# Optimization experiments

Measured on AMD Instinct MI355X. Metric: run time of the kernel, lower is better.

The kernel has to match this reference:

```python
import jax, jax.numpy as jnp
import numpy as np

N = 131072
MANO_CHILD = (2, 3, 17, 5, 6, 18, 8, 9, 20, 11, 12, 19, 14, 15, 16)
MANO_PARENT = (1, 2, 3, 4, 5, 6, 7, 8, 9, 10, 11, 12, 13, 14, 15)
FINGERS = ((0, 1, 2, 3, 17), (0, 4, 5, 6, 18), (0, 7, 8, 9, 20), (0, 10, 11, 12, 19), (0, 13, 14, 15, 16))
PALM = np.array([0, 1, 4, 7, 10, 13])
MAX_FLEX = float(np.pi / 2)  # flexion clamp range [0, pi/2]
EPS = 1e-8


def _wrist_rot(src, dst):
    """Kabsch rotation R (N,3,3) such that R @ src_k ~= dst_k (palm alignment)."""
    H = jnp.einsum('nki,nkj->nij', src, dst)          # sum_k src dst^T
    U, S, Vt = jnp.linalg.svd(H, full_matrices=False)
    VUt = jnp.einsum('nji,nkj->nik', Vt, U)           # V @ U^T
    d = jnp.linalg.det(VUt)
    D = jnp.stack([jnp.ones_like(d), jnp.ones_like(d), d], axis=-1)
    return jnp.einsum('nji,nj,nkj->nik', Vt, D, U)    # V diag(1,1,d) U^T


def _rodrigues(v, axis, theta):
    """Rotate vectors v (N,3) about unit axis (N,3) by angle theta (N,)."""
    c = jnp.cos(theta)[:, None]
    s = jnp.sin(theta)[:, None]
    return v * c + jnp.cross(axis, v) * s + axis * jnp.sum(axis * v, -1, keepdims=True) * (1.0 - c)


def _forward(joints, tempJ):
    wrist = joints[:, :1]
    J = joints - wrist                       # wrist-centered observed joints
    T = tempJ - tempJ[:, :1]                 # wrist-centered template
    bone_ref = T                             # bonelenTempJ: reference bone lengths
    # rigid palm alignment of template onto observed joints
    R = _wrist_rot(T[:, PALM], J[:, PALM])
    T = jnp.einsum('nij,nkj->nki', R, T)     # rotate every template joint
    # palm joints of observation are replaced by aligned template palm
    J = J.at[:, PALM].set(T[:, PALM])
    # (hand-pose-legitimize layer approximated as identity; source unavailable)
    for idx in range(len(MANO_CHILD)):
        ch, pa = MANO_CHILD[idx], MANO_PARENT[idx]
        v1 = J[:, ch] - T[:, pa]
        dis = jnp.linalg.norm(v1, axis=1)
        univ1 = v1 / (dis[:, None] + EPS)
        blen = jnp.linalg.norm(bone_ref[:, ch] - bone_ref[:, pa], axis=1)
        lo, hi = blen, blen                  # non-RHD template: lower == upper
        valid = (lo <= dis) & (dis <= hi)
        clamped = jnp.clip(dis, lo, hi)
        new = jnp.where(valid[:, None], J[:, ch], T[:, pa] + univ1 * clamped[:, None])
        T = T.at[:, ch].set(new)
        # flexion legitimization: clamp bend angle of this bone vs its parent bone
        f = FINGERS[idx // 3]
        k = idx % 3
        gp, pp, cc = f[k], f[k + 1], f[k + 2]  # grandparent, parent(=pa), child(=ch)
        v0 = T[:, pp] - T[:, gp]
        vb = T[:, cc] - T[:, pp]
        cr = jnp.cross(v0, vb)
        s = jnp.linalg.norm(cr, axis=1)
        c = jnp.sum(v0 * vb, axis=1)
        ang = jnp.arctan2(s, c)
        delta = jnp.clip(ang, 0.0, MAX_FLEX) - ang
        axis = cr / (s[:, None] + EPS)
        T = T.at[:, cc].set(_rodrigues(vb, axis, delta) + T[:, pp])
    return wrist + T


def setup_inputs() -> dict:
    key = jax.random.key(0)
    k1, k2 = jax.random.split(key)
    joints = jax.random.normal(k1, (N, 21, 3), dtype=jnp.float32)
    tempJ = jax.random.normal(k2, (N, 21, 3), dtype=jnp.float32)
    return {"joints": joints, "tempJ": tempJ}


def reference(joints, tempJ):
    return _forward(joints, tempJ)
```

## Files before the change

kernel.cpp:

```cpp
#include <hip/hip_runtime.h>
#include <math.h>

#define BLOCK 256
#define HF 63
#define TILE_F (BLOCK * HF)
#define TILE_V4 (TILE_F / 4)

__device__ __forceinline__ float rsqf(float x)  { return __builtin_amdgcn_rsqf(x); }
__device__ __forceinline__ float sqtf(float x)  { return __builtin_amdgcn_sqrtf(x); }

__global__ __launch_bounds__(BLOCK, 2)
void kin_fwd(const float* __restrict__ joints,
             const float* __restrict__ tempJ,
             float* __restrict__ out,
             int n_total)
{
    constexpr int CHILD[15]  = {2,3,17, 5,6,18, 8,9,20, 11,12,19, 14,15,16};
    constexpr int PARENT[15] = {1,2,3, 4,5,6, 7,8,9, 10,11,12, 13,14,15};
    constexpr int GPID[15]   = {0,1,2, 0,4,5, 0,7,8, 0,10,11, 0,13,14};
    constexpr int PALM[6]    = {0,1,4,7,10,13};

    __shared__ float lds[TILE_F];

    const int tid = threadIdx.x;
    const int n   = blockIdx.x * BLOCK + tid;
    const long long tileBase = (long long)blockIdx.x * TILE_F;
    const long long totalF   = (long long)n_total * HF;
    const bool fullTile = (tileBase + TILE_F) <= totalF;
    const bool active = (n < n_total);

    if (fullTile) {
        const float4* g4 = (const float4*)(tempJ + tileBase);
        float4* l4 = (float4*)lds;
        for (int idx = tid; idx < TILE_V4; idx += BLOCK) l4[idx] = g4[idx];
    } else {
        for (int idx = tid; idx < TILE_F; idx += BLOCK) {
            const long long g = tileBase + idx;
            lds[idx] = (g < totalF) ? tempJ[g] : 0.f;
        }
    }
    __syncthreads();

    float T[21][3];
    float blen2[15];

    if (active) {
        const float* tl = lds + tid * HF;
#pragma unroll
        for (int k = 0; k < 21; ++k) {
            T[k][0] = tl[3*k+0];
            T[k][1] = tl[3*k+1];
            T[k][2] = tl[3*k+2];
        }
        const float ox = T[0][0], oy = T[0][1], oz = T[0][2];
#pragma unroll
        for (int k = 0; k < 21; ++k) { T[k][0] -= ox; T[k][1] -= oy; T[k][2] -= oz; }

#pragma unroll
        for (int i = 0; i < 15; ++i) {
            const float dx = T[CHILD[i]][0] - T[PARENT[i]][0];
            const float dy = T[CHILD[i]][1] - T[PARENT[i]][1];
            const float dz = T[CHILD[i]][2] - T[PARENT[i]][2];
            blen2[i] = dx*dx + dy*dy + dz*dz;
        }
    }
    __syncthreads();

    if (fullTile) {
        const float4* g4 = (const float4*)(joints + tileBase);
        float4* l4 = (float4*)lds;
        for (int idx = tid; idx < TILE_V4; idx += BLOCK) l4[idx] = g4[idx];
    } else {
        for (int idx = tid; idx < TILE_F; idx += BLOCK) {
            const long long g = tileBase + idx;
            lds[idx] = (g < totalF) ? joints[g] : 0.f;
        }
    }
    __syncthreads();

    float wx = 0.f, wy = 0.f, wz = 0.f;

    if (active) {
        float Jl[21][3];
        {
            const float* jl = lds + tid * HF;
            wx = jl[0]; wy = jl[1]; wz = jl[2];
#pragma unroll
            for (int k = 0; k < 21; ++k) {
                Jl[k][0] = jl[3*k+0] - wx;
                Jl[k][1] = jl[3*k+1] - wy;
                Jl[k][2] = jl[3*k+2] - wz;
            }
        }

        float H[3][3] = {{0.f,0.f,0.f},{0.f,0.f,0.f},{0.f,0.f,0.f}};
#pragma unroll
        for (int p = 0; p < 6; ++p) {
            const int k = PALM[p];
#pragma unroll
            for (int i = 0; i < 3; ++i)
#pragma unroll
                for (int j = 0; j < 3; ++j)
                    H[i][j] += T[k][i] * Jl[k][j];
        }

        float A[3][3];
#pragma unroll
        for (int i = 0; i < 3; ++i)
#pragma unroll
            for (int j = 0; j < 3; ++j)
                A[i][j] = H[0][i]*H[0][j] + H[1][i]*H[1][j] + H[2][i]*H[2][j];

        const float q   = (A[0][0] + A[1][1] + A[2][2]) * (1.f/3.f);
        const float a00 = A[0][0]-q, a11 = A[1][1]-q, a22 = A[2][2]-q;
        const float a01 = A[0][1], a02 = A[0][2], a12 = A[1][2];
        const float p1  = a01*a01 + a02*a02 + a12*a12;
        const float p2s = a00*a00 + a11*a11 + a22*a22 + 2.f*p1;
        const float p26 = p2s*(1.f/6.f) + 1e-30f;
        const float ip  = rsqf(p26);
        const float p   = p26 * ip;
        const float detC =
            a00*(a11*a22 - a12*a12) - a01*(a01*a22 - a12*a02) + a02*(a01*a12 - a11*a02);
        float r = 0.5f * detC * ip*ip*ip;
        r = fminf(1.f, fmaxf(-1.f, r));
        const float phi_rev = acosf(r) * 0.05305164769729845f;
        const float cph = __builtin_amdgcn_cosf(phi_rev);
        const float sph = __builtin_amdgcn_sinf(phi_rev);
        const float e1 = q + 2.f*p*cph;
        const float e3 = q - p*(cph + 1.7320508075688772f*sph);
        const float e2 = 3.f*q - e1 - e3;

        const float gap12 = e1 - e2, gap23 = e2 - e3;
        const bool isoTop = (gap12 >= gap23);
        const float sAB = isoTop ? (e2 + e3) : (e1 + e2);
        const float pAB = isoTop ? (e2 * e3) : (e1 * e2);

        const float A2_00 = A[0][0]*A[0][0] + A[0][1]*A[0][1] + A[0][2]*A[0][2];
        const float A2_01 = A[0][0]*A[0][1] + A[0][1]*A[1][1] + A[0][2]*A[1][2];
        const float A2_02 = A[0][0]*A[0][2] + A[0][1]*A[1][2] + A[0][2]*A[2][2];
        const float A2_11 = A[0][1]*A[0][1] + A[1][1]*A[1][1] + A[1][2]*A[1][2];
        const float A2_12 = A[0][1]*A[0][2] + A[1][1]*A[1][2] + A[1][2]*A[2][2];
        const float A2_22 = A[0][2]*A[0][2] + A[1][2]*A[1][2] + A[2][2]*A[2][2];

        const float m00 = A2_00 - sAB*A[0][0] + pAB;
        const float m01 = A2_01 - sAB*A[0][1];
        const float m02 = A2_02 - sAB*A[0][2];
        const float m11 = A2_11 - sAB*A[1][1] + pAB;
        const float m12 = A2_12 - sAB*A[1][2];
        const float m22 = A2_22 - sAB*A[2][2] + pAB;

        const float n0c = m00*m00 + m01*m01 + m02*m02;
        const float n1c = m01*m01 + m11*m11 + m12*m12;
        const float n2c = m02*m02 + m12*m12 + m22*m22;
        float vx = m00, vy = m01, vz = m02, nb = n0c;
        if (n1c > nb) { vx = m01; vy = m11; vz = m12; nb = n1c; }
        if (n2c > nb) { vx = m02; vy = m12; vz = m22; nb = n2c; }
        if (nb < 1e-24f) { vx = 1.f; vy = 0.f; vz = 0.f; }
        {
            const float invv = rsqf(vx*vx + vy*vy + vz*vz + 1e-35f);
            vx *= invv; vy *= invv; vz *= invv;
        }

        float hx, hy, hz;
        {
            const float axv = fabsf(vx), ayv = fabsf(vy), azv = fabsf(vz);
            if (axv <= ayv && axv <= azv)      { hx = 0.f;  hy = vz;  hz = -vy; }
            else if (ayv <= azv)               { hx = -vz;  hy = 0.f; hz = vx;  }
            else                               { hx = vy;   hy = -vx; hz = 0.f; }
        }
        const float invh = rsqf(hx*hx + hy*hy + hz*hz + 1e-35f);
        const float b1x = hx*invh, b1y = hy*invh, b1z = hz*invh;
        const float b2x = vy*b1z - vz*b1y;
        const float b2y = vz*b1x - vx*b1z;
        const float b2z = vx*b1y - vy*b1x;

        const float Ab1x = A[0][0]*b1x + A[0][1]*b1y + A[0][2]*b1z;
        const float Ab1y = A[0][1]*b1x + A[1][1]*b1y + A[1][2]*b1z;
        const float Ab1z = A[0][2]*b1x + A[1][2]*b1y + A[2][2]*b1z;
        const float Ab2x = A[0][0]*b2x + A[0][1]*b2y + A[0][2]*b2z;
        const float Ab2y = A[0][1]*b2x + A[1][1]*b2y + A[1][2]*b2z;
        const float Ab2z = A[0][2]*b2x + A[1][2]*b2y + A[2][2]*b2z;
        const float alpha = b1x*Ab1x + b1y*Ab1y + b1z*Ab1z;
        const float beta  = b2x*Ab1x + b2y*Ab1y + b2z*Ab1z;
        const float gamma = b2x*Ab2x + b2y*Ab2y + b2z*Ab2z;

        const float difq  = 0.5f*(alpha - gamma);
        const float rootq = sqtf(difq*difq + beta*beta);
        float tx = beta, ty = rootq - difq;
        if (tx*tx + ty*ty < 1e-30f) { tx = 1.f; ty = 0.f; }
        const float invt = rsqf(tx*tx + ty*ty + 1e-35f);
        const float ctx = tx*invt, cty = ty*invt;
        const float wpx = ctx*b1x + cty*b2x;
        const float wpy = ctx*b1y + cty*b2y;
        const float wpz = ctx*b1z + cty*b2z;
        const float wmx = vy*wpz - vz*wpy;
        const float wmy = vz*wpx - vx*wpz;
        const float wmz = vx*wpy - vy*wpx;

        const float v1x = isoTop ? vx  : wpx;
        const float v1y = isoTop ? vy  : wpy;
        const float v1z = isoTop ? vz  : wpz;
        const float v2x = isoTop ? wpx : wmx;
        const float v2y = isoTop ? wpy : wmy;
        const float v2z = isoTop ? wpz : wmz;
        const float v3x = v1y*v2z - v1z*v2y;
        const float v3y = v1z*v2x - v1x*v2z;
        const float v3z = v1x*v2y - v1y*v2x;

        float R[3][3];
        {
            const float w1x = H[0][0]*v1x + H[0][1]*v1y + H[0][2]*v1z;
            const float w1y = H[1][0]*v1x + H[1][1]*v1y + H[1][2]*v1z;
            const float w1z = H[2][0]*v1x + H[2][1]*v1y + H[2][2]*v1z;
            const float in1 = rsqf(w1x*w1x + w1y*w1y + w1z*w1z + 1e-35f);
            const float u1x = w1x*in1, u1y = w1y*in1, u1z = w1z*in1;

            float w2x = H[0][0]*v2x + H[0][1]*v2y + H[0][2]*v2z;
            float w2y = H[1][0]*v2x + H[1][1]*v2y + H[1][2]*v2z;
            float w2z = H[2][0]*v2x + H[2][1]*v2y + H[2][2]*v2z;
            const float dp = u1x*w2x + u1y*w2y + u1z*w2z;
            w2x -= dp*u1x; w2y -= dp*u1y; w2z -= dp*u1z;
            const float in2 = rsqf(w2x*w2x + w2y*w2y + w2z*w2z + 1e-35f);
            const float u2x = w2x*in2, u2y = w2y*in2, u2z = w2z*in2;

            const float u3x = u1y*u2z - u1z*u2y;
            const float u3y = u1z*u2x - u1x*u2z;
            const float u3z = u1x*u2y - u1y*u2x;

            R[0][0] = v1x*u1x + v2x*u2x + v3x*u3x;
            R[0][1] = v1x*u1y + v2x*u2y + v3x*u3y;
            R[0][2] = v1x*u1z + v2x*u2z + v3x*u3z;
            R[1][0] = v1y*u1x + v2y*u2x + v3y*u3x;
            R[1][1] = v1y*u1y + v2y*u2y + v3y*u3y;
            R[1][2] = v1y*u1z + v2y*u2z + v3y*u3z;
            R[2][0] = v1z*u1x + v2z*u2x + v3z*u3x;
            R[2][1] = v1z*u1y + v2z*u2y + v3z*u3y;
            R[2][2] = v1z*u1z + v2z*u2z + v3z*u3z;
        }

#pragma unroll
        for (int k = 0; k < 21; ++k) {
            const float x = T[k][0], y = T[k][1], z = T[k][2];
            T[k][0] = R[0][0]*x + R[0][1]*y + R[0][2]*z;
            T[k][1] = R[1][0]*x + R[1][1]*y + R[1][2]*z;
            T[k][2] = R[2][0]*x + R[2][1]*y + R[2][2]*z;
        }

#pragma unroll
        for (int i = 0; i < 15; ++i) {
            const int ch = CHILD[i], pa = PARENT[i], gp = GPID[i];

            const float v1xc = Jl[ch][0] - T[pa][0];
            const float v1yc = Jl[ch][1] - T[pa][1];
            const float v1zc = Jl[ch][2] - T[pa][2];
            const float d2  = v1xc*v1xc + v1yc*v1yc + v1zc*v1zc;
            const float b2  = blen2[i];
            const float sc  = b2 * rsqf(b2*d2 + 1e-30f);
            const float vbx = v1xc*sc, vby = v1yc*sc, vbz = v1zc*sc;

            const float v0x = T[pa][0] - T[gp][0];
            const float v0y = T[pa][1] - T[gp][1];
            const float v0z = T[pa][2] - T[gp][2];

            const float crx = v0y*vbz - v0z*vby;
            const float cry = v0z*vbx - v0x*vbz;
            const float crz = v0x*vby - v0y*vbx;
            const float s2  = crx*crx + cry*cry + crz*crz;
            const float c   = v0x*vbx + v0y*vby + v0z*vbz;

            const float invr  = rsqf(s2 + c*c + 1e-35f);
            const float sainv = rsqf(s2 + 1e-35f);
            const float s     = s2 * sainv;
            const float cosd  = (c < 0.f) ? s*invr : 1.f;
            const float sind  = (c < 0.f) ? c*invr : 0.f;

            const float ax = crx*sainv, ay = cry*sainv, az = crz*sainv;
            const float cxx = ay*vbz - az*vby;
            const float cxy = az*vbx - ax*vbz;
            const float cxz = ax*vby - ay*vbx;
            T[ch][0] = vbx*cosd + cxx*sind + T[pa][0];
            T[ch][1] = vby*cosd + cxy*sind + T[pa][1];
            T[ch][2] = vbz*cosd + cxz*sind + T[pa][2];
        }

        float* ol = lds + tid * HF;
#pragma unroll
        for (int k = 0; k < 21; ++k) {
            ol[3*k+0] = wx + T[k][0];
            ol[3*k+1] = wy + T[k][1];
            ol[3*k+2] = wz + T[k][2];
        }
    }
    __syncthreads();

    if (fullTile) {
        float4* g4 = (float4*)(out + tileBase);
        const float4* l4 = (const float4*)lds;
        for (int idx = tid; idx < TILE_V4; idx += BLOCK) g4[idx] = l4[idx];
    } else {
        for (int idx = tid; idx < TILE_F; idx += BLOCK) {
            const long long g = tileBase + idx;
            if (g < totalF) out[g] = lds[idx];
        }
    }
}

extern "C" void kernel_launch(void* const* d_in, const int* in_sizes, int n_in,
                              void* d_out, int out_size, void* d_ws, size_t ws_size,
                              hipStream_t stream)
{
    const float* joints = (const float*)d_in[0];
    const float* tempJ  = (const float*)d_in[1];
    float* out          = (float*)d_out;

    const int n_total = in_sizes[0] / 63;
    const int grid = (n_total + BLOCK - 1) / BLOCK;
    kin_fwd<<<grid, BLOCK, 0, stream>>>(joints, tempJ, out, n_total);
}
```

Measured before the change: 110.5 us.

## Prefetch joints tile into registers and read joints from LDS on demand

The joints tile is now loaded into registers (16 float4 per thread) at the same time as the tempJ tile goes to LDS, so both global loads are in flight together instead of being serialized behind a barrier. Observed joints are read from LDS when needed instead of being copied into a 63-float register array. The palm covariance skips the wrist joint, which is always zero after centering. The bone loop is reordered to interleave the five independent fingers for more ILP. The changes add register pressure from the prefetch buffer, which could hurt occupancy at launch bounds of 2 blocks per SIMD, and add more LDS reads.

```diff
diff --git a/kernel.cpp b/kernel.cpp
--- a/kernel.cpp
+++ b/kernel.cpp
@@ -18,7 +18,7 @@
     constexpr int CHILD[15]  = {2,3,17, 5,6,18, 8,9,20, 11,12,19, 14,15,16};
     constexpr int PARENT[15] = {1,2,3, 4,5,6, 7,8,9, 10,11,12, 13,14,15};
     constexpr int GPID[15]   = {0,1,2, 0,4,5, 0,7,8, 0,10,11, 0,13,14};
-    constexpr int PALM[6]    = {0,1,4,7,10,13};
+    constexpr int PALMNZ[5]  = {1,4,7,10,13};
 
     __shared__ float lds[TILE_F];
 
@@ -29,10 +29,21 @@
     const bool fullTile = (tileBase + TILE_F) <= totalF;
     const bool active = (n < n_total);
 
+    float4 jr[16];
     if (fullTile) {
-        const float4* g4 = (const float4*)(tempJ + tileBase);
+        const float4* gt = (const float4*)(tempJ + tileBase);
+        const float4* gj = (const float4*)(joints + tileBase);
         float4* l4 = (float4*)lds;
-        for (int idx = tid; idx < TILE_V4; idx += BLOCK) l4[idx] = g4[idx];
+#pragma unroll
+        for (int r = 0; r < 16; ++r) {
+            const int idx = r * BLOCK + tid;
+            if (idx < TILE_V4) l4[idx] = gt[idx];
+        }
+#pragma unroll
+        for (int r = 0; r < 16; ++r) {
+            const int idx = r * BLOCK + tid;
+            if (idx < TILE_V4) jr[r] = gj[idx];
+        }
     } else {
         for (int idx = tid; idx < TILE_F; idx += BLOCK) {
             const long long g = tileBase + idx;
@@ -67,9 +78,12 @@
     __syncthreads();
 
     if (fullTile) {
-        const float4* g4 = (const float4*)(joints + tileBase);
         float4* l4 = (float4*)lds;
-        for (int idx = tid; idx < TILE_V4; idx += BLOCK) l4[idx] = g4[idx];
+#pragma unroll
+        for (int r = 0; r < 16; ++r) {
+            const int idx = r * BLOCK + tid;
+            if (idx < TILE_V4) l4[idx] = jr[r];
+        }
     } else {
         for (int idx = tid; idx < TILE_F; idx += BLOCK) {
             const long long g = tileBase + idx;
@@ -81,27 +95,18 @@
     float wx = 0.f, wy = 0.f, wz = 0.f;
 
     if (active) {
-        float Jl[21][3];
-        {
-            const float* jl = lds + tid * HF;
-            wx = jl[0]; wy = jl[1]; wz = jl[2];
-#pragma unroll
-            for (int k = 0; k < 21; ++k) {
-                Jl[k][0] = jl[3*k+0] - wx;
-                Jl[k][1] = jl[3*k+1] - wy;
-                Jl[k][2] = jl[3*k+2] - wz;
-            }
-        }
+        const float* jl = lds + tid * HF;
+        wx = jl[0]; wy = jl[1]; wz = jl[2];
+        #define JLC(k,d) (jl[3*(k)+(d)] - ((d)==0 ? wx : ((d)==1 ? wy : wz)))
 
         float H[3][3] = {{0.f,0.f,0.f},{0.f,0.f,0.f},{0.f,0.f,0.f}};
 #pragma unroll
-        for (int p = 0; p < 6; ++p) {
-            const int k = PALM[p];
-#pragma unroll
-            for (int i = 0; i < 3; ++i)
-#pragma unroll
-                for (int j = 0; j < 3; ++j)
-                    H[i][j] += T[k][i] * Jl[k][j];
+        for (int p = 0; p < 5; ++p) {
+            const int k = PALMNZ[p];
+            const float jx = JLC(k,0), jy = JLC(k,1), jz = JLC(k,2);
+            H[0][0] += T[k][0]*jx; H[0][1] += T[k][0]*jy; H[0][2] += T[k][0]*jz;
+            H[1][0] += T[k][1]*jx; H[1][1] += T[k][1]*jy; H[1][2] += T[k][1]*jz;
+            H[2][0] += T[k][2]*jx; H[2][1] += T[k][2]*jy; H[2][2] += T[k][2]*jz;
         }
 
         float A[3][3];
@@ -247,41 +252,46 @@
         }
 
 #pragma unroll
-        for (int i = 0; i < 15; ++i) {
-            const int ch = CHILD[i], pa = PARENT[i], gp = GPID[i];
-
-            const float v1xc = Jl[ch][0] - T[pa][0];
-            const float v1yc = Jl[ch][1] - T[pa][1];
-            const float v1zc = Jl[ch][2] - T[pa][2];
-            const float d2  = v1xc*v1xc + v1yc*v1yc + v1zc*v1zc;
-            const float b2  = blen2[i];
-            const float sc  = b2 * rsqf(b2*d2 + 1e-30f);
-            const float vbx = v1xc*sc, vby = v1yc*sc, vbz = v1zc*sc;
-
-            const float v0x = T[pa][0] - T[gp][0];
-            const float v0y = T[pa][1] - T[gp][1];
-            const float v0z = T[pa][2] - T[gp][2];
-
-            const float crx = v0y*vbz - v0z*vby;
-            const float cry = v0z*vbx - v0x*vbz;
-            const float crz = v0x*vby - v0y*vbx;
-            const float s2  = crx*crx + cry*cry + crz*crz;
-            const float c   = v0x*vbx + v0y*vby + v0z*vbz;
-
-            const float invr  = rsqf(s2 + c*c + 1e-35f);
-            const float sainv = rsqf(s2 + 1e-35f);
-            const float s     = s2 * sainv;
-            const float cosd  = (c < 0.f) ? s*invr : 1.f;
-            const float sind  = (c < 0.f) ? c*invr : 0.f;
-
-            const float ax = crx*sainv, ay = cry*sainv, az = crz*sainv;
-            const float cxx = ay*vbz - az*vby;
-            const float cxy = az*vbx - ax*vbz;
-            const float cxz = ax*vby - ay*vbx;
-            T[ch][0] = vbx*cosd + cxx*sind + T[pa][0];
-            T[ch][1] = vby*cosd + cxy*sind + T[pa][1];
-            T[ch][2] = vbz*cosd + cxz*sind + T[pa][2];
-        }
+        for (int k2 = 0; k2 < 3; ++k2) {
+#pragma unroll
+            for (int f = 0; f < 5; ++f) {
+                const int i = f*3 + k2;
+                const int ch = CHILD[i], pa = PARENT[i], gp = GPID[i];
+
+                const float v1xc = JLC(ch,0) - T[pa][0];
+                const float v1yc = JLC(ch,1) - T[pa][1];
+                const float v1zc = JLC(ch,2) - T[pa][2];
+                const float d2  = v1xc*v1xc + v1yc*v1yc + v1zc*v1zc;
+                const float b2  = blen2[i];
+                const float sc  = b2 * rsqf(b2*d2 + 1e-30f);
+                const float vbx = v1xc*sc, vby = v1yc*sc, vbz = v1zc*sc;
+
+                const float v0x = T[pa][0] - T[gp][0];
+                const float v0y = T[pa][1] - T[gp][1];
+                const float v0z = T[pa][2] - T[gp][2];
+
+                const float crx = v0y*vbz - v0z*vby;
+                const float cry = v0z*vbx - v0x*vbz;
+                const float crz = v0x*vby - v0y*vbx;
+                const float s2  = crx*crx + cry*cry + crz*crz;
+                const float c   = v0x*vbx + v0y*vby + v0z*vbz;
+
+                const float invr  = rsqf(s2 + c*c + 1e-35f);
+                const float sainv = rsqf(s2 + 1e-35f);
+                const float s     = s2 * sainv;
+                const float cosd  = (c < 0.f) ? s*invr : 1.f;
+                const float sind  = (c < 0.f) ? c*invr : 0.f;
+
+                const float ax = crx*sainv, ay = cry*sainv, az = crz*sainv;
+                const float cxx = ay*vbz - az*vby;
+                const float cxy = az*vbx - ax*vbz;
+                const float cxz = ax*vby - ay*vbx;
+                T[ch][0] = vbx*cosd + cxx*sind + T[pa][0];
+                T[ch][1] = vby*cosd + cxy*sind + T[pa][1];
+                T[ch][2] = vbz*cosd + cxz*sind + T[pa][2];
+            }
+        }
+        #undef JLC
 
         float* ol = lds + tid * HF;
 #pragma unroll
```

New measurement: 119.8 us. 1.08x slower.
